# Kernel optimization log

Hardware: AMD Instinct MI355X
Metric: run time of the kernel (lower is better)

## Reference

```python
import jax, jax.numpy as jnp
import numpy as np

N = 100000      # number of nodes
FT = 256        # ft_in (hidden units)
NB_CLASSES = 16 # nb_classes
EPS = 1e-8      # torch.cosine_similarity eps


def setup_inputs() -> dict:
    key = jax.random.key(0)
    ks = jax.random.split(key, 7)
    seq = jax.random.normal(ks[0], (N, FT), dtype=jnp.float32)
    seq1 = jax.random.normal(ks[1], (N, FT), dtype=jnp.float32)
    labels = jax.random.randint(ks[2], (N,), 0, NB_CLASSES, dtype=jnp.int32)
    prompt1 = jax.random.normal(ks[3], (1, FT), dtype=jnp.float32)
    prompt2 = jax.random.normal(ks[4], (1, FT), dtype=jnp.float32)
    prompt3 = jax.random.normal(ks[5], (1, FT), dtype=jnp.float32)
    # weighted_prompt.reset_parameters: fixed init 0.5, 0.4, 0.3
    w_wp = jnp.array([[0.5, 0.4, 0.3]], dtype=jnp.float32)
    # weighted_feature.reset_parameters: fixed init 0.0, 1.0
    w_wf = jnp.array([[0.0, 1.0]], dtype=jnp.float32)
    # downstreamprompt.weight: xavier_uniform on [1, ft_in]
    bound = float(np.sqrt(6.0 / (1 + FT)))
    w_dp = jax.random.uniform(ks[6], (1, FT), jnp.float32, -bound, bound)
    a4 = jnp.array([0.1], dtype=jnp.float32)
    return {"seq": seq, "seq1": seq1, "labels": labels,
            "prompt1": prompt1, "prompt2": prompt2, "prompt3": prompt3,
            "w_wp": w_wp, "w_wf": w_wf, "w_dp": w_dp, "a4": a4}


def reference(seq, seq1, labels, prompt1, prompt2, prompt3, w_wp, w_wf, w_dp, a4):
    # weight = 1 + ELU(weighted_prompt(prompt))  -> [1, FT]
    prompt = jnp.concatenate([prompt1, prompt2, prompt3], axis=0)  # [3, FT]
    weight = 1.0 + jax.nn.elu(w_wp @ prompt)                       # [1, FT]
    rawret1 = weight * seq                                          # [N, FT]
    rawret2 = w_dp * seq                                            # downstreamprompt
    rawret3 = jax.nn.elu(w_wf[0, 0] * rawret1 + w_wf[0, 1] * rawret2)
    rawret = rawret3 + a4[0] * seq1                                 # [N, FT]
    # averageemb (train=1 path): per-class mean, zero-count classes stay 0
    sums = jax.ops.segment_sum(rawret, labels, num_segments=NB_CLASSES)  # [C, FT]
    counts = jax.ops.segment_sum(jnp.ones((rawret.shape[0],), rawret.dtype),
                                 labels, num_segments=NB_CLASSES)        # [C]
    ave = jnp.where(counts[:, None] > 0, sums / jnp.maximum(counts, 1.0)[:, None], sums)
    # fused per-pair cosine similarity: normalize + matmul (replaces N*C loop)
    num = rawret @ ave.T                                             # [N, C]
    denom = (jnp.linalg.norm(rawret, axis=1)[:, None] *
             jnp.linalg.norm(ave, axis=1)[None, :])
    ret = num / jnp.maximum(denom, EPS)
    return jax.nn.softmax(ret, axis=1)
```

## Files before the change

### kernel.cpp

```cpp
#include <hip/hip_runtime.h>
#include <hip/hip_bf16.h>

#define NROWS 100000
#define FT 256
#define NC 16
#define NBLK 512
#define NSL 8
#define SLICE (NBLK / NSL)

#define FPSCALE 1048576.0f
#define FPINV   (1.0f / 1048576.0f)

#define CW_AVEB 0
#define CW_NRM  2048
#define CW_PCNT 2064
#define CW_ST2C (CW_PCNT + NBLK*NC)
#define CW_ST2  (CW_ST2C + NSL*NC)
#define CW_PART (CW_ST2 + NSL*NC*FT)
#define CW_RAWB (CW_PART + NBLK*NC*FT)
#define CW_TOTAL (CW_RAWB + (NROWS*FT)/2)
#define CACHED_NEED_BYTES ((size_t)CW_TOTAL * 4)

#define WS_COEF 0
#define WS_SUMS 256
#define WS_CNTS 4352
#define WS_AVEB 4368
#define WS_NRM  6416

typedef float f32x4 __attribute__((ext_vector_type(4)));
typedef short bf16x8 __attribute__((ext_vector_type(8)));

static __device__ __forceinline__ float bfbits2f(unsigned int u16) {
    union { unsigned int i; float f; } v; v.i = u16 << 16; return v.f;
}
static __device__ __forceinline__ unsigned short f2bf(float f) {
    union { float f; unsigned int i; } v; v.f = f;
    unsigned int u = v.i;
    u += 0x7fffu + ((u >> 16) & 1u);
    return (unsigned short)(u >> 16);
}


__global__ __launch_bounds__(1024) void k_accum_c(
    const float* __restrict__ seq,
    const float* __restrict__ seq1,
    const int* __restrict__ labels,
    const float* __restrict__ p1,
    const float* __restrict__ p2,
    const float* __restrict__ p3,
    const float* __restrict__ wwp,
    const float* __restrict__ wwf,
    const float* __restrict__ wdp,
    const float* __restrict__ a4p,
    float* __restrict__ ws)
{
    __shared__ int lsum[NC * FT];
    __shared__ int lcnt[NC];
    __shared__ __align__(16) float scoef[FT];
    const int tid = threadIdx.x;
    for (int i = tid; i < NC * FT; i += 1024) lsum[i] = 0;
    if (tid < NC) lcnt[tid] = 0;
    if (tid < FT) {
        float z = wwp[0] * p1[tid] + wwp[1] * p2[tid] + wwp[2] * p3[tid];
        float w = (z > 0.f) ? (1.f + z) : __expf(z);
        scoef[tid] = wwf[0] * w + wwf[1] * wdp[tid];
    }
    __syncthreads();

    const int rr = tid >> 5;
    const int m  = tid & 31;
    const int f0 = m * 8;
    const int mh = m >> 2;
    int off[8];
#pragma unroll
    for (int i = 0; i < 8; ++i) off[i] = (i + mh) & 7;

    float cof[8];
    {
        const float4 c0 = *(const float4*)(scoef + f0);
        const float4 c1 = *(const float4*)(scoef + f0 + 4);
        cof[0]=c0.x; cof[1]=c0.y; cof[2]=c0.z; cof[3]=c0.w;
        cof[4]=c1.x; cof[5]=c1.y; cof[6]=c1.z; cof[7]=c1.w;
    }
    const float a4v = a4p[0];
    unsigned int* rawb = (unsigned int*)(ws + CW_RAWB);

    const int stride = NBLK * 32;
    for (int rowA = blockIdx.x * 32 + rr; rowA < NROWS; rowA += stride * 2) {
        const int rowBr = rowA + stride;
        const bool vB = rowBr < NROWS;
        const int rowB = vB ? rowBr : rowA;
        const int labA = labels[rowA];
        const int labB = labels[rowB];
        const float4 saA = *(const float4*)(seq  + rowA * FT + f0);
        const float4 sbA = *(const float4*)(seq  + rowA * FT + f0 + 4);
        const float4 taA = *(const float4*)(seq1 + rowA * FT + f0);
        const float4 tbA = *(const float4*)(seq1 + rowA * FT + f0 + 4);
        const float4 saB = *(const float4*)(seq  + rowB * FT + f0);
        const float4 sbB = *(const float4*)(seq  + rowB * FT + f0 + 4);
        const float4 taB = *(const float4*)(seq1 + rowB * FT + f0);
        const float4 tbB = *(const float4*)(seq1 + rowB * FT + f0 + 4);

        const float sA[8] = {saA.x,saA.y,saA.z,saA.w, sbA.x,sbA.y,sbA.z,sbA.w};
        const float tA[8] = {taA.x,taA.y,taA.z,taA.w, tbA.x,tbA.y,tbA.z,tbA.w};
        const float sB[8] = {saB.x,saB.y,saB.z,saB.w, sbB.x,sbB.y,sbB.z,sbB.w};
        const float tB[8] = {taB.x,taB.y,taB.z,taB.w, tbB.x,tbB.y,tbB.z,tbB.w};

        int* baseA = lsum + labA * FT + f0;
        unsigned short vbA[8];
#pragma unroll
        for (int i = 0; i < 8; ++i) {
            float u = cof[i] * sA[i];
            float r = (u > 0.f) ? u : (__expf(u) - 1.f);
            float v = r + a4v * tA[i];
            vbA[i] = f2bf(v);
            atomicAdd(baseA + off[i], __float2int_rn(v * FPSCALE));
        }
        uint4 pkA;
        pkA.x = (unsigned int)vbA[0] | ((unsigned int)vbA[1] << 16);
        pkA.y = (unsigned int)vbA[2] | ((unsigned int)vbA[3] << 16);
        pkA.z = (unsigned int)vbA[4] | ((unsigned int)vbA[5] << 16);
        pkA.w = (unsigned int)vbA[6] | ((unsigned int)vbA[7] << 16);
        *(uint4*)(rawb + (rowA * FT + f0) / 2) = pkA;
        if (m == 0) atomicAdd(&lcnt[labA], 1);

        int* baseB = lsum + labB * FT + f0;
        unsigned short vbB[8];
        float vv[8];
#pragma unroll
        for (int i = 0; i < 8; ++i) {
            float u = cof[i] * sB[i];
            float r = (u > 0.f) ? u : (__expf(u) - 1.f);
            vv[i] = r + a4v * tB[i];
            vbB[i] = f2bf(vv[i]);
        }
        if (vB) {
#pragma unroll
            for (int i = 0; i < 8; ++i)
                atomicAdd(baseB + off[i], __float2int_rn(vv[i] * FPSCALE));
            uint4 pkB;
            pkB.x = (unsigned int)vbB[0] | ((unsigned int)vbB[1] << 16);
            pkB.y = (unsigned int)vbB[2] | ((unsigned int)vbB[3] << 16);
            pkB.z = (unsigned int)vbB[4] | ((unsigned int)vbB[5] << 16);
            pkB.w = (unsigned int)vbB[6] | ((unsigned int)vbB[7] << 16);
            *(uint4*)(rawb + (rowB * FT + f0) / 2) = pkB;
            if (m == 0) atomicAdd(&lcnt[labB], 1);
        }
    }
    __syncthreads();

    int* gpart = (int*)(ws + CW_PART) + blockIdx.x * (NC * FT);
    for (int idx = tid; idx < NC * FT; idx += 1024) {
        int p  = idx & 255;
        int mm = p >> 3;
        int r  = p & 7;
        int f  = (p & ~7) | ((r - (mm >> 2)) & 7);
        gpart[(idx & ~255) + f] = lsum[idx];
    }
    if (tid < NC) ((int*)(ws + CW_PCNT))[blockIdx.x * NC + tid] = lcnt[tid];
}

__global__ __launch_bounds__(256) void k_reduce1(float* __restrict__ ws)
{
    const int c = blockIdx.x >> 3;
    const int r = blockIdx.x & 7;
    const int f = threadIdx.x;
    const int p0 = r * SLICE;
    const int* gpart = (const int*)(ws + CW_PART);
    int acc = 0;
#pragma unroll
    for (int p = 0; p < SLICE; ++p)
        acc += gpart[(p0 + p) * (NC * FT) + c * FT + f];
    ((int*)(ws + CW_ST2))[(r * NC + c) * FT + f] = acc;

    if (f < SLICE) {
        int cc = ((const int*)(ws + CW_PCNT))[(p0 + f) * NC + c];
#pragma unroll
        for (int o = 32; o > 0; o >>= 1) cc += __shfl_down(cc, o, 64);
        if (f == 0) ((int*)(ws + CW_ST2C))[r * NC + c] = cc;
    }
}

__global__ __launch_bounds__(256) void k_reduce2(float* __restrict__ ws)
{
    __shared__ float red[256];
    const int c = blockIdx.x;
    const int f = threadIdx.x;
    const int* st2  = (const int*)(ws + CW_ST2);
    const int* st2c = (const int*)(ws + CW_ST2C);
    long long isum = 0;
    int cnt = 0;
#pragma unroll
    for (int s = 0; s < NSL; ++s) {
        isum += (long long)st2[(s * NC + c) * FT + f];
        cnt  += st2c[s * NC + c];
    }
    float a = ((float)isum * FPINV) / fmaxf((float)cnt, 1.f);
    unsigned short ab = f2bf(a);
    ((unsigned short*)(ws + CW_AVEB))[c * FT + f] = ab;
    float af = bfbits2f(ab);

    red[f] = af * af;
    __syncthreads();
#pragma unroll
    for (int s = 128; s > 0; s >>= 1) {
        if (f < s) red[f] += red[f + s];
        __syncthreads();
    }
    if (f == 0) ws[CW_NRM + c] = sqrtf(red[0]);
}

__global__ __launch_bounds__(256) void k_out_c(
    const float* __restrict__ ws,
    float* __restrict__ out)
{
    const int tid = threadIdx.x;
    const int lane = tid & 63;
    const int wv   = tid >> 6;
    const int c = lane & 15;
    const int g = lane >> 4;

    const unsigned short* aveb = (const unsigned short*)(ws + CW_AVEB);
    const unsigned short* rawb = (const unsigned short*)(ws + CW_RAWB);
    bf16x8 bfrag[8];
#pragma unroll
    for (int kc = 0; kc < 8; ++kc)
        bfrag[kc] = *(const bf16x8*)(aveb + c * FT + kc * 32 + g * 8);
    const float na = ws[CW_NRM + c];

    const int ntiles = NROWS / 16;
    for (int tile = blockIdx.x * 4 + wv; tile < ntiles; tile += gridDim.x * 4) {
        const int rowbase = tile * 16;
        const int arow = rowbase + c;
        f32x4 accC = {0.f, 0.f, 0.f, 0.f};
        f32x4 accS = {0.f, 0.f, 0.f, 0.f};
#pragma unroll
        for (int kc = 0; kc < 8; ++kc) {
            bf16x8 afrag = *(const bf16x8*)(rawb + arow * FT + kc * 32 + g * 8);
            accC = __builtin_amdgcn_mfma_f32_16x16x32_bf16(afrag, bfrag[kc], accC, 0, 0, 0);
            accS = __builtin_amdgcn_mfma_f32_16x16x32_bf16(afrag, afrag,     accS, 0, 0, 0);
        }
#pragma unroll
        for (int q = 0; q < 4; ++q) {
            const float sd = __shfl(accS[q], g * 20 + q, 64);
            const float nr = sqrtf(fmaxf(sd, 0.f));
            const float denom = fmaxf(nr * na, 1e-8f);
            float cosv = accC[q] / denom;
            float mx = cosv;
#pragma unroll
            for (int o = 1; o < 16; o <<= 1) mx = fmaxf(mx, __shfl_xor(mx, o, 16));
            const float e = __expf(cosv - mx);
            float s = e;
#pragma unroll
            for (int o = 1; o < 16; o <<= 1) s += __shfl_xor(s, o, 16);
            out[(rowbase + g * 4 + q) * NC + c] = e / s;
        }
    }
}


__global__ void k_prep(const float* __restrict__ p1,
                       const float* __restrict__ p2,
                       const float* __restrict__ p3,
                       const float* __restrict__ wwp,
                       const float* __restrict__ wwf,
                       const float* __restrict__ wdp,
                       float* __restrict__ ws)
{
    int f = threadIdx.x;
    float z = wwp[0] * p1[f] + wwp[1] * p2[f] + wwp[2] * p3[f];
    float weight = (z > 0.f) ? (1.f + z) : __expf(z);
    ws[WS_COEF + f] = wwf[0] * weight + wwf[1] * wdp[f];
}

__global__ __launch_bounds__(1024) void k_accum(
    const float* __restrict__ seq,
    const float* __restrict__ seq1,
    const int* __restrict__ labels,
    const float* __restrict__ a4p,
    float* __restrict__ ws)
{
    __shared__ int lsum[NC * FT];
    __shared__ int lcnt[NC];
    const int tid = threadIdx.x;
    for (int i = tid; i < NC * FT; i += 1024) lsum[i] = 0;
    if (tid < NC) lcnt[tid] = 0;
    __syncthreads();

    const int rr = tid >> 5;
    const int m  = tid & 31;
    const int f0 = m * 8;
    const int mh = m >> 2;
    int off[8];
#pragma unroll
    for (int i = 0; i < 8; ++i) off[i] = (i + mh) & 7;

    float cof[8];
    {
        const float4 c0 = *(const float4*)(ws + WS_COEF + f0);
        const float4 c1 = *(const float4*)(ws + WS_COEF + f0 + 4);
        cof[0]=c0.x; cof[1]=c0.y; cof[2]=c0.z; cof[3]=c0.w;
        cof[4]=c1.x; cof[5]=c1.y; cof[6]=c1.z; cof[7]=c1.w;
    }
    const float a4v = a4p[0];

    for (int row = blockIdx.x * 32 + rr; row < NROWS; row += gridDim.x * 32) {
        const int lab = labels[row];
        const float4 sa  = *(const float4*)(seq  + row * FT + f0);
        const float4 sb  = *(const float4*)(seq  + row * FT + f0 + 4);
        const float4 ta  = *(const float4*)(seq1 + row * FT + f0);
        const float4 tb  = *(const float4*)(seq1 + row * FT + f0 + 4);
        const float s[8]  = {sa.x,sa.y,sa.z,sa.w, sb.x,sb.y,sb.z,sb.w};
        const float t[8]  = {ta.x,ta.y,ta.z,ta.w, tb.x,tb.y,tb.z,tb.w};
        int* base = lsum + lab * FT + f0;
#pragma unroll
        for (int i = 0; i < 8; ++i) {
            float u = cof[i] * s[i];
            float r = (u > 0.f) ? u : (__expf(u) - 1.f);
            atomicAdd(base + off[i], __float2int_rn((r + a4v * t[i]) * FPSCALE));
        }
        if (m == 0) atomicAdd(&lcnt[lab], 1);
    }
    __syncthreads();

    int* gsum = (int*)(ws + WS_SUMS);
    for (int idx = tid; idx < NC * FT; idx += 1024) {
        int p  = idx & 255;
        int mm = p >> 3;
        int r  = p & 7;
        int f  = (p & ~7) | ((r - (mm >> 2)) & 7);
        atomicAdd(gsum + (idx & ~255) + f, lsum[idx]);
    }
    if (tid < NC) atomicAdd((int*)(ws + WS_CNTS) + tid, lcnt[tid]);
}

__global__ void k_final(float* __restrict__ ws)
{
    __shared__ float nacc[NC];
    const int f = threadIdx.x;
    if (f < NC) nacc[f] = 0.f;
    __syncthreads();
    const int* gsum = (const int*)(ws + WS_SUMS);
    const int* gcnt = (const int*)(ws + WS_CNTS);
    unsigned short* aveb = (unsigned short*)(ws + WS_AVEB);
#pragma unroll
    for (int c = 0; c < NC; ++c) {
        float cnt = (float)gcnt[c];
        float a = ((float)gsum[c * FT + f] * FPINV) / fmaxf(cnt, 1.f);
        unsigned short ab = f2bf(a);
        aveb[c * FT + f] = ab;
        float af = bfbits2f(ab);
        atomicAdd(&nacc[c], af * af);
    }
    __syncthreads();
    if (f < NC) ws[WS_NRM + f] = sqrtf(nacc[f]);
}

__global__ __launch_bounds__(256) void k_out(
    const float* __restrict__ seq,
    const float* __restrict__ seq1,
    const float* __restrict__ a4p,
    const float* __restrict__ ws,
    float* __restrict__ out)
{
    __shared__ __align__(16) float scoef[FT];
    const int tid = threadIdx.x;
    for (int i = tid; i < FT; i += 256) scoef[i] = ws[WS_COEF + i];
    __syncthreads();

    const int lane = tid & 63;
    const int wv   = tid >> 6;
    const int c = lane & 15;
    const int g = lane >> 4;

    const unsigned short* aveb = (const unsigned short*)(ws + WS_AVEB);
    bf16x8 bfrag[8];
#pragma unroll
    for (int kc = 0; kc < 8; ++kc)
        bfrag[kc] = *(const bf16x8*)(aveb + c * FT + kc * 32 + g * 8);
    const float na  = ws[WS_NRM + c];
    const float a4v = a4p[0];

    const int ntiles = NROWS / 16;
    for (int tile = blockIdx.x * 4 + wv; tile < ntiles; tile += gridDim.x * 4) {
        const int rowbase = tile * 16;
        const int arow = rowbase + c;
        f32x4 accC = {0.f, 0.f, 0.f, 0.f};
        f32x4 accS = {0.f, 0.f, 0.f, 0.f};
#pragma unroll
        for (int kc = 0; kc < 8; ++kc) {
            const int k0 = kc * 32 + g * 8;
            const float4 sa = *(const float4*)(seq  + arow * FT + k0);
            const float4 sb = *(const float4*)(seq  + arow * FT + k0 + 4);
            const float4 ta = *(const float4*)(seq1 + arow * FT + k0);
            const float4 tb = *(const float4*)(seq1 + arow * FT + k0 + 4);
            const float4 c0 = *(const float4*)(scoef + k0);
            const float4 c1 = *(const float4*)(scoef + k0 + 4);
            const float s[8]  = {sa.x,sa.y,sa.z,sa.w, sb.x,sb.y,sb.z,sb.w};
            const float t[8]  = {ta.x,ta.y,ta.z,ta.w, tb.x,tb.y,tb.z,tb.w};
            const float cf[8] = {c0.x,c0.y,c0.z,c0.w, c1.x,c1.y,c1.z,c1.w};
            bf16x8 afrag;
#pragma unroll
            for (int i = 0; i < 8; ++i) {
                float u = cf[i] * s[i];
                float r = (u > 0.f) ? u : (__expf(u) - 1.f);
                afrag[i] = (short)f2bf(r + a4v * t[i]);
            }
            accC = __builtin_amdgcn_mfma_f32_16x16x32_bf16(afrag, bfrag[kc], accC, 0, 0, 0);
            accS = __builtin_amdgcn_mfma_f32_16x16x32_bf16(afrag, afrag,     accS, 0, 0, 0);
        }
#pragma unroll
        for (int q = 0; q < 4; ++q) {
            const float sd = __shfl(accS[q], g * 20 + q, 64);
            const float nr = sqrtf(fmaxf(sd, 0.f));
            const float denom = fmaxf(nr * na, 1e-8f);
            float cosv = accC[q] / denom;
            float mx = cosv;
#pragma unroll
            for (int o = 1; o < 16; o <<= 1) mx = fmaxf(mx, __shfl_xor(mx, o, 16));
            const float e = __expf(cosv - mx);
            float s = e;
#pragma unroll
            for (int o = 1; o < 16; o <<= 1) s += __shfl_xor(s, o, 16);
            out[(rowbase + g * 4 + q) * NC + c] = e / s;
        }
    }
}

extern "C" void kernel_launch(void* const* d_in, const int* in_sizes, int n_in,
                              void* d_out, int out_size, void* d_ws, size_t ws_size,
                              hipStream_t stream)
{
    const float* seq  = (const float*)d_in[0];
    const float* seq1 = (const float*)d_in[1];
    const int*   lab  = (const int*)d_in[2];
    const float* p1   = (const float*)d_in[3];
    const float* p2   = (const float*)d_in[4];
    const float* p3   = (const float*)d_in[5];
    const float* wwp  = (const float*)d_in[6];
    const float* wwf  = (const float*)d_in[7];
    const float* wdp  = (const float*)d_in[8];
    const float* a4   = (const float*)d_in[9];
    float* ws  = (float*)d_ws;
    float* out = (float*)d_out;

    if (ws_size >= CACHED_NEED_BYTES) {
        k_accum_c<<<NBLK,    1024, 0, stream>>>(seq, seq1, lab, p1, p2, p3,
                                                wwp, wwf, wdp, a4, ws);
        k_reduce1<<<NC * NSL, 256, 0, stream>>>(ws);
        k_reduce2<<<NC,       256, 0, stream>>>(ws);
        k_out_c  <<<1568,     256, 0, stream>>>(ws, out);
    } else {
        hipMemsetAsync((char*)d_ws + WS_SUMS * sizeof(int), 0,
                       (NC * FT + NC) * sizeof(int), stream);
        k_prep <<<1,    256, 0, stream>>>(p1, p2, p3, wwp, wwf, wdp, ws);
        k_accum<<<512, 1024, 0, stream>>>(seq, seq1, lab, a4, ws);
        k_final<<<1,    256, 0, stream>>>(ws);
        k_out  <<<1568, 256, 0, stream>>>(seq, seq1, a4, ws, out);
    }
}
```

Measured before the change: 269.8 us.

## Replace LDS atomic class sums with per-wave register accumulators

The accumulation kernel now gives each 64-lane wave a whole row (4 features per lane) and keeps a per-class float accumulator for every class in registers. Each lane adds its values into all classes with a 0/1 mask taken from the wave-uniform label, which removes the shared-memory integer atomics. Waves are then combined through LDS in sequence and converted to fixed point only once per block. The block drops to 256 threads. The cost is 16x redundant FMAs, 64 accumulator registers per lane, and a float summation order that differs from the earlier exact integer sums.

```diff
diff --git a/kernel.cpp b/kernel.cpp
--- a/kernel.cpp
+++ b/kernel.cpp
@@ -41,7 +41,7 @@
 }
 
 
-__global__ __launch_bounds__(1024) void k_accum_c(
+__global__ __launch_bounds__(256) void k_accum_c(
     const float* __restrict__ seq,
     const float* __restrict__ seq1,
     const int* __restrict__ labels,
@@ -54,110 +54,110 @@
     const float* __restrict__ a4p,
     float* __restrict__ ws)
 {
-    __shared__ int lsum[NC * FT];
-    __shared__ int lcnt[NC];
     __shared__ __align__(16) float scoef[FT];
+    __shared__ __align__(16) float lsumf[NC * FT];
+    __shared__ int lcnti[4 * NC];
     const int tid = threadIdx.x;
-    for (int i = tid; i < NC * FT; i += 1024) lsum[i] = 0;
-    if (tid < NC) lcnt[tid] = 0;
-    if (tid < FT) {
+
+    {
         float z = wwp[0] * p1[tid] + wwp[1] * p2[tid] + wwp[2] * p3[tid];
         float w = (z > 0.f) ? (1.f + z) : __expf(z);
         scoef[tid] = wwf[0] * w + wwf[1] * wdp[tid];
     }
     __syncthreads();
 
-    const int rr = tid >> 5;
-    const int m  = tid & 31;
-    const int f0 = m * 8;
-    const int mh = m >> 2;
-    int off[8];
-#pragma unroll
-    for (int i = 0; i < 8; ++i) off[i] = (i + mh) & 7;
-
-    float cof[8];
+    const int wv = tid >> 6;
+    const int l  = tid & 63;
+    const int fl = l * 4;
+
+    float cof[4];
     {
-        const float4 c0 = *(const float4*)(scoef + f0);
-        const float4 c1 = *(const float4*)(scoef + f0 + 4);
-        cof[0]=c0.x; cof[1]=c0.y; cof[2]=c0.z; cof[3]=c0.w;
-        cof[4]=c1.x; cof[5]=c1.y; cof[6]=c1.z; cof[7]=c1.w;
+        const float4 c4 = *(const float4*)(scoef + fl);
+        cof[0] = c4.x; cof[1] = c4.y; cof[2] = c4.z; cof[3] = c4.w;
     }
     const float a4v = a4p[0];
     unsigned int* rawb = (unsigned int*)(ws + CW_RAWB);
 
-    const int stride = NBLK * 32;
-    for (int rowA = blockIdx.x * 32 + rr; rowA < NROWS; rowA += stride * 2) {
-        const int rowBr = rowA + stride;
-        const bool vB = rowBr < NROWS;
-        const int rowB = vB ? rowBr : rowA;
-        const int labA = labels[rowA];
-        const int labB = labels[rowB];
-        const float4 saA = *(const float4*)(seq  + rowA * FT + f0);
-        const float4 sbA = *(const float4*)(seq  + rowA * FT + f0 + 4);
-        const float4 taA = *(const float4*)(seq1 + rowA * FT + f0);
-        const float4 tbA = *(const float4*)(seq1 + rowA * FT + f0 + 4);
-        const float4 saB = *(const float4*)(seq  + rowB * FT + f0);
-        const float4 sbB = *(const float4*)(seq  + rowB * FT + f0 + 4);
-        const float4 taB = *(const float4*)(seq1 + rowB * FT + f0);
-        const float4 tbB = *(const float4*)(seq1 + rowB * FT + f0 + 4);
-
-        const float sA[8] = {saA.x,saA.y,saA.z,saA.w, sbA.x,sbA.y,sbA.z,sbA.w};
-        const float tA[8] = {taA.x,taA.y,taA.z,taA.w, tbA.x,tbA.y,tbA.z,tbA.w};
-        const float sB[8] = {saB.x,saB.y,saB.z,saB.w, sbB.x,sbB.y,sbB.z,sbB.w};
-        const float tB[8] = {taB.x,taB.y,taB.z,taB.w, tbB.x,tbB.y,tbB.z,tbB.w};
-
-        int* baseA = lsum + labA * FT + f0;
-        unsigned short vbA[8];
-#pragma unroll
-        for (int i = 0; i < 8; ++i) {
-            float u = cof[i] * sA[i];
-            float r = (u > 0.f) ? u : (__expf(u) - 1.f);
-            float v = r + a4v * tA[i];
-            vbA[i] = f2bf(v);
-            atomicAdd(baseA + off[i], __float2int_rn(v * FPSCALE));
-        }
-        uint4 pkA;
-        pkA.x = (unsigned int)vbA[0] | ((unsigned int)vbA[1] << 16);
-        pkA.y = (unsigned int)vbA[2] | ((unsigned int)vbA[3] << 16);
-        pkA.z = (unsigned int)vbA[4] | ((unsigned int)vbA[5] << 16);
-        pkA.w = (unsigned int)vbA[6] | ((unsigned int)vbA[7] << 16);
-        *(uint4*)(rawb + (rowA * FT + f0) / 2) = pkA;
-        if (m == 0) atomicAdd(&lcnt[labA], 1);
-
-        int* baseB = lsum + labB * FT + f0;
-        unsigned short vbB[8];
-        float vv[8];
-#pragma unroll
-        for (int i = 0; i < 8; ++i) {
-            float u = cof[i] * sB[i];
-            float r = (u > 0.f) ? u : (__expf(u) - 1.f);
-            vv[i] = r + a4v * tB[i];
-            vbB[i] = f2bf(vv[i]);
-        }
-        if (vB) {
-#pragma unroll
-            for (int i = 0; i < 8; ++i)
-                atomicAdd(baseB + off[i], __float2int_rn(vv[i] * FPSCALE));
-            uint4 pkB;
-            pkB.x = (unsigned int)vbB[0] | ((unsigned int)vbB[1] << 16);
-            pkB.y = (unsigned int)vbB[2] | ((unsigned int)vbB[3] << 16);
-            pkB.z = (unsigned int)vbB[4] | ((unsigned int)vbB[5] << 16);
-            pkB.w = (unsigned int)vbB[6] | ((unsigned int)vbB[7] << 16);
-            *(uint4*)(rawb + (rowB * FT + f0) / 2) = pkB;
-            if (m == 0) atomicAdd(&lcnt[labB], 1);
-        }
-    }
-    __syncthreads();
+    float acc[NC][4];
+#pragma unroll
+    for (int c = 0; c < NC; ++c)
+#pragma unroll
+        for (int i = 0; i < 4; ++i) acc[c][i] = 0.f;
+    int scnt[NC];
+#pragma unroll
+    for (int c = 0; c < NC; ++c) scnt[c] = 0;
+
+    const int wg = blockIdx.x * 4 + wv;
+    const int NQ = NROWS / 4;
+    for (int q = wg; q < NQ; q += NBLK * 4) {
+        const int r0 = q * 4;
+        int lb[4]; float4 s4[4], t4[4];
+#pragma unroll
+        for (int j = 0; j < 4; ++j) {
+            lb[j] = labels[r0 + j];
+            s4[j] = *(const float4*)(seq  + (r0 + j) * FT + fl);
+            t4[j] = *(const float4*)(seq1 + (r0 + j) * FT + fl);
+        }
+#pragma unroll
+        for (int j = 0; j < 4; ++j) {
+            const float ss[4] = {s4[j].x, s4[j].y, s4[j].z, s4[j].w};
+            const float tt[4] = {t4[j].x, t4[j].y, t4[j].z, t4[j].w};
+            float v[4];
+#pragma unroll
+            for (int i = 0; i < 4; ++i) {
+                float u = cof[i] * ss[i];
+                float r = (u > 0.f) ? u : (__expf(u) - 1.f);
+                v[i] = r + a4v * tt[i];
+            }
+            uint2 pk;
+            pk.x = (unsigned int)f2bf(v[0]) | ((unsigned int)f2bf(v[1]) << 16);
+            pk.y = (unsigned int)f2bf(v[2]) | ((unsigned int)f2bf(v[3]) << 16);
+            *(uint2*)(rawb + ((r0 + j) * FT + fl) / 2) = pk;
+            const int ls = __builtin_amdgcn_readfirstlane(lb[j]);
+#pragma unroll
+            for (int c = 0; c < NC; ++c) {
+                const float m = (ls == c) ? 1.0f : 0.0f;
+#pragma unroll
+                for (int i = 0; i < 4; ++i)
+                    acc[c][i] = fmaf(m, v[i], acc[c][i]);
+                scnt[c] += (ls == c) ? 1 : 0;
+            }
+        }
+    }
+
+    if (l == 0) {
+#pragma unroll
+        for (int c = 0; c < NC; ++c) lcnti[wv * NC + c] = scnt[c];
+    }
+
+    for (int w = 0; w < 4; ++w) {
+        if (wv == w) {
+#pragma unroll
+            for (int c = 0; c < NC; ++c) {
+                float4* p = (float4*)(lsumf + c * FT + fl);
+                if (w == 0) {
+                    float4 nv; nv.x = acc[c][0]; nv.y = acc[c][1];
+                    nv.z = acc[c][2]; nv.w = acc[c][3];
+                    *p = nv;
+                } else {
+                    float4 old = *p;
+                    old.x += acc[c][0]; old.y += acc[c][1];
+                    old.z += acc[c][2]; old.w += acc[c][3];
+                    *p = old;
+                }
+            }
+        }
+        __syncthreads();
+    }
 
     int* gpart = (int*)(ws + CW_PART) + blockIdx.x * (NC * FT);
-    for (int idx = tid; idx < NC * FT; idx += 1024) {
-        int p  = idx & 255;
-        int mm = p >> 3;
-        int r  = p & 7;
-        int f  = (p & ~7) | ((r - (mm >> 2)) & 7);
-        gpart[(idx & ~255) + f] = lsum[idx];
-    }
-    if (tid < NC) ((int*)(ws + CW_PCNT))[blockIdx.x * NC + tid] = lcnt[tid];
+    for (int idx = tid; idx < NC * FT; idx += 256)
+        gpart[idx] = __float2int_rn(lsumf[idx] * FPSCALE);
+    if (tid < NC) {
+        int cc = lcnti[tid] + lcnti[NC + tid] + lcnti[2 * NC + tid]
+               + lcnti[3 * NC + tid];
+        ((int*)(ws + CW_PCNT))[blockIdx.x * NC + tid] = cc;
+    }
 }
 
 __global__ __launch_bounds__(256) void k_reduce1(float* __restrict__ ws)
@@ -445,7 +445,7 @@
     float* out = (float*)d_out;
 
     if (ws_size >= CACHED_NEED_BYTES) {
-        k_accum_c<<<NBLK,    1024, 0, stream>>>(seq, seq1, lab, p1, p2, p3,
+        k_accum_c<<<NBLK,     256, 0, stream>>>(seq, seq1, lab, p1, p2, p3,
                                                 wwp, wwf, wdp, a4, ws);
         k_reduce1<<<NC * NSL, 256, 0, stream>>>(ws);
         k_reduce2<<<NC,       256, 0, stream>>>(ws);
```

New measurement: 267.9 us. No clear change (-0.7%).
